# Performance work log

Hardware: AMD Instinct MI355X
Metric: run time of the kernel (lower is better)

Reference implementation:

```python
import jax, jax.numpy as jnp
import numpy as np

N_NODES = 100000
N_EDGES = 1600000
F_IN = 128
F_HID = 128
F_OUT = 128
N_GRAPHS = 256


def setup_inputs() -> dict:
    key = jax.random.key(0)
    ks = jax.random.split(key, 8)
    x = jax.random.normal(ks[0], (N_NODES, F_IN), dtype=jnp.float32)
    edge_index = jax.random.randint(ks[1], (2, N_EDGES), 0, N_NODES, dtype=jnp.int64)
    batch = jnp.sort(jax.random.randint(ks[2], (N_NODES,), 0, N_GRAPHS, dtype=jnp.int64))
    W1 = jax.random.normal(ks[3], (F_IN, F_HID), dtype=jnp.float32) * 0.05
    b1 = jax.random.normal(ks[4], (F_HID,), dtype=jnp.float32) * 0.05
    W2 = jax.random.normal(ks[5], (F_HID, F_OUT), dtype=jnp.float32) * 0.05
    b2 = jax.random.normal(ks[6], (F_OUT,), dtype=jnp.float32) * 0.05
    return {"x": x, "edge_index": edge_index, "batch": batch,
            "W1": W1, "b1": b1, "W2": W2, "b2": b2}


def reference(x, edge_index, batch, W1, b1, W2, b2):
    n = x.shape[0]
    # --- GCNConv (PyG defaults: add self-loops, symmetric normalization) ---
    loop = jnp.arange(n, dtype=edge_index.dtype)
    row = jnp.concatenate([edge_index[0], loop])  # source nodes
    col = jnp.concatenate([edge_index[1], loop])  # target nodes
    ones = jnp.ones_like(col, dtype=x.dtype)
    deg = jax.ops.segment_sum(ones, col, num_segments=n)          # in-degree incl. self-loop
    dinv = jnp.where(deg > 0, jax.lax.rsqrt(deg), 0.0)
    norm = dinv[row] * dinv[col]                                  # [E+N]
    h = x @ W1                                                    # transform first (PyG order)
    msg = h[row] * norm[:, None]                                  # gather + normalize
    agg = jax.ops.segment_sum(msg, col, num_segments=n) + b1      # scatter-add + bias
    h = jax.nn.relu(agg)
    # --- global_mean_pool over graphs ---
    g_ones = jnp.ones((n,), dtype=x.dtype)
    cnt = jax.ops.segment_sum(g_ones, batch, num_segments=N_GRAPHS)
    pooled = jax.ops.segment_sum(h, batch, num_segments=N_GRAPHS)
    pooled = pooled / jnp.clip(cnt, 1.0)[:, None]
    # --- linear + tanh ---
    return jnp.tanh(pooled @ W2 + b2)
```

## Files before the change

kernel.cpp:

```cpp
#include <hip/hip_runtime.h>
#include <math.h>

#define F 128
#define N_GRAPHS 256
#define BK_SHIFT 8
#define BK_NODES 256
#define BK_CAP 6144
#define MAXBK 512
#define SC_CAP 3200
#define NSCAT 512

typedef __attribute__((ext_vector_type(4))) float f32x4;
typedef __attribute__((ext_vector_type(2))) float f32x2;
typedef __attribute__((ext_vector_type(8))) short bf16x8;
typedef __attribute__((ext_vector_type(8))) unsigned short u16x8;

__device__ __forceinline__ unsigned short f2bf(float f) {
    unsigned u = __float_as_uint(f);
    unsigned r = (u + 0x7FFFu + ((u >> 16) & 1u)) >> 16;
    return (unsigned short)r;
}
__device__ __forceinline__ float bf2f(unsigned short u) {
    return __uint_as_float(((unsigned)u) << 16);
}
__device__ __forceinline__ int idxval(const int* raw, int i, bool is32) {
    return is32 ? raw[i] : (int)((const long long*)raw)[i];
}

#if defined(__has_builtin)
#if __has_builtin(__builtin_amdgcn_cvt_pk_f32_fp8) && __has_builtin(__builtin_amdgcn_cvt_pk_fp8_f32)
#define HW_FP8 1
#endif
#endif

__device__ __forceinline__ unsigned char f2fp8(float f) {
#ifdef HW_FP8
    int p = __builtin_amdgcn_cvt_pk_fp8_f32(f, f, 0, false);
    return (unsigned char)(p & 0xFF);
#else
    float a = fabsf(f);
    unsigned s = (f < 0.f) ? 0x80u : 0u;
    if (a >= 448.f) return s | 0x7E;
    if (a < 0.015625f) {
        int m = (int)(a * 512.f + 0.5f);
        return s | (unsigned)m;
    }
    int ex;
    float fr = frexpf(a, &ex);
    int e = ex - 1;
    int q = (int)(a * exp2f((float)(3 - e)) + 0.5f) - 8;
    if (q == 8) { q = 0; e += 1; }
    return s | ((unsigned)(e + 7) << 3) | (unsigned)q;
#endif
}

__device__ __forceinline__ void fp8x16_fma(uint4 v, float w, float* acc) {
#ifdef HW_FP8
    f32x2 p;
    p = __builtin_amdgcn_cvt_pk_f32_fp8((int)v.x, false); acc[0]  += w * p[0]; acc[1]  += w * p[1];
    p = __builtin_amdgcn_cvt_pk_f32_fp8((int)v.x, true);  acc[2]  += w * p[0]; acc[3]  += w * p[1];
    p = __builtin_amdgcn_cvt_pk_f32_fp8((int)v.y, false); acc[4]  += w * p[0]; acc[5]  += w * p[1];
    p = __builtin_amdgcn_cvt_pk_f32_fp8((int)v.y, true);  acc[6]  += w * p[0]; acc[7]  += w * p[1];
    p = __builtin_amdgcn_cvt_pk_f32_fp8((int)v.z, false); acc[8]  += w * p[0]; acc[9]  += w * p[1];
    p = __builtin_amdgcn_cvt_pk_f32_fp8((int)v.z, true);  acc[10] += w * p[0]; acc[11] += w * p[1];
    p = __builtin_amdgcn_cvt_pk_f32_fp8((int)v.w, false); acc[12] += w * p[0]; acc[13] += w * p[1];
    p = __builtin_amdgcn_cvt_pk_f32_fp8((int)v.w, true);  acc[14] += w * p[0]; acc[15] += w * p[1];
#else
    unsigned ww[4] = {v.x, v.y, v.z, v.w};
#pragma unroll
    for (int j = 0; j < 16; ++j) {
        unsigned b = (ww[j >> 2] >> ((j & 3) * 8)) & 0xFF;
        int e = (b >> 3) & 0xF, m = b & 7;
        float val = e ? ldexpf((float)(8 + m), e - 10) : ldexpf((float)m, -9);
        acc[j] += (b & 0x80) ? -(w * val) : (w * val);
    }
#endif
}

__global__ __launch_bounds__(256) void scatter_gemm_kernel(
    const int* __restrict__ ei_raw, int nE,
    const int* __restrict__ batch_raw, int nN,
    const float* __restrict__ x, const float* __restrict__ W1,
    unsigned char* __restrict__ h_f8,
    int* __restrict__ bcursor, int2* __restrict__ tmp, int nBk) {
    extern __shared__ char smem[];
    int t = threadIdx.x;

    if (blockIdx.x < NSCAT) {
        int2* ebuf  = (int2*)smem;
        int*  hist  = (int*)(smem + SC_CAP * 8);
        int*  rbase = hist + MAXBK;
        bool is32 = (batch_raw[nN - 1] != 0);
        int cs = (nE + NSCAT - 1) / NSCAT;
        int e0 = blockIdx.x * cs;
        int e1 = min(nE, e0 + cs);

        for (int s0 = e0; s0 < e1; s0 += SC_CAP) {
            int m = min(SC_CAP, e1 - s0);
            for (int i = t; i < nBk; i += 256) hist[i] = 0;
            __syncthreads();
            for (int i = t; i < m; i += 256) {
                int r = idxval(ei_raw, s0 + i, is32);
                int c = idxval(ei_raw, nE + s0 + i, is32);
                ebuf[i] = make_int2(r, c);
                atomicAdd(&hist[c >> BK_SHIFT], 1);
            }
            __syncthreads();
            for (int i = t; i < nBk; i += 256) {
                int hv = hist[i];
                rbase[i] = hv ? (i * BK_CAP + atomicAdd(&bcursor[i], hv)) : 0;
                hist[i] = 0;
            }
            __syncthreads();
            for (int i = t; i < m; i += 256) {
                int2 e = ebuf[i];
                int b = e.y >> BK_SHIFT;
                int pos = rbase[b] + atomicAdd(&hist[b], 1);
                if (pos < (b + 1) * BK_CAP)
                    tmp[pos] = e;
            }
            __syncthreads();
        }
    } else {
        unsigned short* xs = (unsigned short*)smem;
        unsigned short* wl = (unsigned short*)(smem + 32768);
        int row0 = (blockIdx.x - NSCAT) * 128;

        for (int cch = t; cch < 2048; cch += 256) {
            int n = cch & 127, kc = cch >> 7;
            u16x8 o;
#pragma unroll
            for (int j = 0; j < 8; ++j) o[j] = f2bf(W1[(kc * 8 + j) * F + n]);
            int byte = (n * 256 + kc * 16) ^ ((n & 7) << 4);
            *(u16x8*)((char*)wl + byte) = o;
        }
#pragma unroll
        for (int j = 0; j < 16; ++j) {
            int idx = t + j * 256;
            int r = idx >> 5, c4 = idx & 31;
            int gr = row0 + r;
            float4 v = make_float4(0.f, 0.f, 0.f, 0.f);
            if (gr < nN) v = ((const float4*)x)[(size_t)gr * 32 + c4];
            ushort4 o;
            o.x = f2bf(v.x); o.y = f2bf(v.y); o.z = f2bf(v.z); o.w = f2bf(v.w);
            int byte = (r * 256 + c4 * 8) ^ ((r & 7) << 4);
            *(ushort4*)((char*)xs + byte) = o;
        }
        __syncthreads();

        int lane = t & 63;
        int w = t >> 6;
        int m0 = (w >> 1) * 64;
        int n0 = (w & 1) * 64;
        int l15 = lane & 15;
        int lg = lane >> 4;

        f32x4 acc[4][4] = {};
#pragma unroll
        for (int ks = 0; ks < 4; ++ks) {
            bf16x8 a[4], b[4];
#pragma unroll
            for (int i = 0; i < 4; ++i) {
                int r = m0 + i * 16 + l15;
                int byte = (r * 256 + ks * 64 + lg * 16) ^ ((r & 7) << 4);
                a[i] = *(const bf16x8*)((const char*)xs + byte);
            }
#pragma unroll
            for (int j = 0; j < 4; ++j) {
                int n = n0 + j * 16 + l15;
                int byte = (n * 256 + ks * 64 + lg * 16) ^ ((n & 7) << 4);
                b[j] = *(const bf16x8*)((const char*)wl + byte);
            }
#pragma unroll
            for (int i = 0; i < 4; ++i)
#pragma unroll
                for (int j = 0; j < 4; ++j)
                    acc[i][j] = __builtin_amdgcn_mfma_f32_16x16x32_bf16(
                        a[i], b[j], acc[i][j], 0, 0, 0);
        }

#pragma unroll
        for (int i = 0; i < 4; ++i) {
#pragma unroll
            for (int r = 0; r < 4; ++r) {
                int gm = row0 + m0 + i * 16 + lg * 4 + r;
                if (gm < nN) {
#pragma unroll
                    for (int j = 0; j < 4; ++j) {
                        int n = n0 + j * 16 + l15;
                        h_f8[(size_t)gm * F + n] = f2fp8(acc[i][j][r]);
                    }
                }
            }
        }
    }
}

__global__ __launch_bounds__(256) void bucket_build_kernel(
    const int2* __restrict__ tmp, const int* __restrict__ bfill, int nN,
    int* __restrict__ off, int* __restrict__ cnt, float* __restrict__ dinv,
    int* __restrict__ csr) {
    __shared__ int2 ebuf[BK_CAP];
    __shared__ int h[BK_NODES];
    __shared__ int pfx[BK_NODES];
    __shared__ int lcur[BK_NODES];
    int b = blockIdx.x;
    int t = threadIdx.x;
    int nodeLo = b << BK_SHIFT;
    int base = b * BK_CAP;
    int m = min(bfill[b], BK_CAP);

    h[t] = 0;
    for (int i = t; i < m; i += 256) ebuf[i] = tmp[base + i];
    __syncthreads();
    for (int i = t; i < m; i += 256)
        atomicAdd(&h[ebuf[i].y - nodeLo], 1);
    __syncthreads();
    int own = h[t];
    int pad = (own + 3) & ~3;
    pfx[t] = pad;
    __syncthreads();
    for (int st = 1; st < 256; st <<= 1) {
        int add = (t >= st) ? pfx[t - st] : 0;
        __syncthreads();
        pfx[t] += add;
        __syncthreads();
    }
    int myoff = base + pfx[t] - pad;
    lcur[t] = myoff;
    int node = nodeLo + t;
    if (node < nN) {
        off[node] = myoff;
        cnt[node] = own;
        dinv[node] = rsqrtf((float)(own + 1));
    }
    __syncthreads();
    for (int i = t; i < m; i += 256) {
        int2 e = ebuf[i];
        int pos = atomicAdd(&lcur[e.y - nodeLo], 1);
        csr[pos] = e.x;
    }
}

__global__ __launch_bounds__(256) void aggregate_kernel(
    const unsigned char* __restrict__ h_f8, const int* __restrict__ csr,
    const int* __restrict__ off, const int* __restrict__ cnt,
    const float* __restrict__ dinv, const float* __restrict__ b1,
    unsigned short* __restrict__ agg_bf, int nN) {
    int t = threadIdx.x;
    int lane = t & 7;
    int c = blockIdx.x * 32 + (t >> 3);
    if (c >= nN) return;

    const uint4* h4 = (const uint4*)h_f8;
    int n = cnt[c];
    float dc = rsqrtf((float)(n + 1));
    float acc[16];
#pragma unroll
    for (int j = 0; j < 16; ++j) acc[j] = 0.f;
    fp8x16_fma(h4[(size_t)c * 8 + lane], dc, acc);

    int lo = off[c];
    int k = 0;
    for (; k + 4 <= n; k += 4) {
        int4 e = *(const int4*)(csr + lo + k);
        float w0 = dinv[e.x];
        float w1 = dinv[e.y];
        float w2 = dinv[e.z];
        float w3 = dinv[e.w];
        uint4 v0 = h4[(size_t)e.x * 8 + lane];
        uint4 v1 = h4[(size_t)e.y * 8 + lane];
        uint4 v2 = h4[(size_t)e.z * 8 + lane];
        uint4 v3 = h4[(size_t)e.w * 8 + lane];
        fp8x16_fma(v0, w0, acc);
        fp8x16_fma(v1, w1, acc);
        fp8x16_fma(v2, w2, acc);
        fp8x16_fma(v3, w3, acc);
    }
    if (k < n) {
        int4 e = *(const int4*)(csr + lo + k);
        fp8x16_fma(h4[(size_t)e.x * 8 + lane], dinv[e.x], acc);
        if (k + 1 < n) fp8x16_fma(h4[(size_t)e.y * 8 + lane], dinv[e.y], acc);
        if (k + 2 < n) fp8x16_fma(h4[(size_t)e.z * 8 + lane], dinv[e.z], acc);
    }

    const float* b1p = b1 + lane * 16;
    u16x8 r0, r1;
#pragma unroll
    for (int j = 0; j < 8; ++j) {
        r0[j] = f2bf(fmaxf(b1p[j] + dc * acc[j], 0.f));
        r1[j] = f2bf(fmaxf(b1p[8 + j] + dc * acc[8 + j], 0.f));
    }
    *(u16x8*)(agg_bf + (size_t)c * F + lane * 16) = r0;
    *(u16x8*)(agg_bf + (size_t)c * F + lane * 16 + 8) = r1;
}

__global__ __launch_bounds__(256) void pool_final_kernel(
    const unsigned short* __restrict__ agg_bf,
    const int* __restrict__ batch_raw, int nN,
    const float* __restrict__ W2, const float* __restrict__ b2,
    float* __restrict__ out) {
    int g = blockIdx.x;
    bool is32 = (batch_raw[nN - 1] != 0);
    __shared__ int bounds[2];
    __shared__ float sd[16][F];
    __shared__ float ps[F];
    int t = threadIdx.x;
    if (t < 2) {
        int target = g + t;
        int lo = 0, hi = nN;
        while (lo < hi) {
            int mid = (lo + hi) >> 1;
            if (idxval(batch_raw, mid, is32) < target) lo = mid + 1; else hi = mid;
        }
        bounds[t] = lo;
    }
    __syncthreads();
    int lo = bounds[0], hi = bounds[1];

    int lane = t & 15;
    int grp = t >> 4;
    const u16x8* a8 = (const u16x8*)agg_bf;
    float acc[8];
#pragma unroll
    for (int j = 0; j < 8; ++j) acc[j] = 0.f;
    for (int n = lo + grp; n < hi; n += 16) {
        u16x8 v = a8[(size_t)n * 16 + lane];
#pragma unroll
        for (int j = 0; j < 8; ++j) acc[j] += bf2f(v[j]);
    }
#pragma unroll
    for (int j = 0; j < 8; ++j) sd[grp][lane * 8 + j] = acc[j];
    __syncthreads();

    if (t < F) {
        float s = 0.f;
#pragma unroll
        for (int i = 0; i < 16; ++i) s += sd[i][t];
        float cntf = (float)(hi - lo);
        ps[t] = s / fmaxf(cntf, 1.0f);
    }
    __syncthreads();

    if (t < F) {
        float s = b2[t];
        for (int k = 0; k < F; ++k) s += ps[k] * W2[k * F + t];
        out[g * F + t] = tanhf(s);
    }
}

extern "C" void kernel_launch(void* const* d_in, const int* in_sizes, int n_in,
                              void* d_out, int out_size, void* d_ws, size_t ws_size,
                              hipStream_t stream) {
    const float* x     = (const float*)d_in[0];
    const int*   ei    = (const int*)d_in[1];
    const int*   batch = (const int*)d_in[2];
    const float* W1    = (const float*)d_in[3];
    const float* b1    = (const float*)d_in[4];
    const float* W2    = (const float*)d_in[5];
    const float* b2    = (const float*)d_in[6];
    float* out = (float*)d_out;

    const int nN = in_sizes[2];
    const int nE = in_sizes[1] / 2;
    const int nBk = (nN + BK_NODES - 1) >> BK_SHIFT;
    const int nGemm = (nN + 127) / 128;

    char* ws = (char*)d_ws;
    size_t woff = 0;
    auto take = [&](size_t bytes) {
        void* p = ws + woff;
        woff += (bytes + 15) & ~(size_t)15;
        return p;
    };
    unsigned char*  h_f8   = (unsigned char*)take((size_t)nN * F);
    unsigned short* agg_bf = (unsigned short*)take((size_t)nN * F * 2);
    int2*  tmp      = (int2*)take((size_t)nBk * BK_CAP * 8);
    int*   csr      = (int*)take((size_t)nBk * BK_CAP * 4);
    int*   cnt      = (int*)take((size_t)nN * 4);
    int*   off      = (int*)take((size_t)nN * 4);
    float* dinv     = (float*)take((size_t)nN * 4);
    int*   bcursor  = (int*)take((size_t)nBk * 4);

    hipMemsetAsync(bcursor, 0, (size_t)nBk * 4, stream);
    scatter_gemm_kernel<<<NSCAT + nGemm, 256, 65536, stream>>>(
        ei, nE, batch, nN, x, W1, h_f8, bcursor, tmp, nBk);
    bucket_build_kernel<<<nBk, 256, 0, stream>>>(tmp, bcursor, nN, off, cnt,
                                                 dinv, csr);
    aggregate_kernel<<<(nN + 31) / 32, 256, 0, stream>>>(h_f8, csr, off, cnt,
                                                         dinv, b1, agg_bf, nN);
    pool_final_kernel<<<N_GRAPHS, 256, 0, stream>>>(agg_bf, batch, nN, W2, b2, out);
}
```

Before: 130.3 us.

## Pack bucketed edges into 32-bit words and pretranspose W1 to bf16 once

Each bucketed edge is now one 32-bit word: the source index in the low 20 bits and the target's offset inside its bucket in the high bits. This halves the temp buffer's global traffic and the LDS footprint in the bucket build kernel. W1 is converted to a transposed bf16 copy once by a small new kernel. GEMM blocks then read their B fragments straight from global/L2 instead of each block rebuilding W1 in shared memory, which halves the dynamic LDS request of the fused kernel. The cost is an extra launch, uncoalesced-ish global B loads, and an assumption that node counts fit in 20 bits.

```diff
diff --git a/kernel.cpp b/kernel.cpp
--- a/kernel.cpp
+++ b/kernel.cpp
@@ -77,12 +77,19 @@
 #endif
 }
 
+__global__ __launch_bounds__(256) void w1t_kernel(
+    const float* __restrict__ W1, unsigned short* __restrict__ W1T) {
+    int i = blockIdx.x * 256 + threadIdx.x;
+    int k = i >> 7, n = i & 127;
+    W1T[n * F + k] = f2bf(W1[i]);
+}
+
 __global__ __launch_bounds__(256) void scatter_gemm_kernel(
     const int* __restrict__ ei_raw, int nE,
     const int* __restrict__ batch_raw, int nN,
-    const float* __restrict__ x, const float* __restrict__ W1,
+    const float* __restrict__ x, const unsigned short* __restrict__ W1T,
     unsigned char* __restrict__ h_f8,
-    int* __restrict__ bcursor, int2* __restrict__ tmp, int nBk) {
+    int* __restrict__ bcursor, int* __restrict__ tmp, int nBk) {
     extern __shared__ char smem[];
     int t = threadIdx.x;
 
@@ -117,23 +124,14 @@
                 int b = e.y >> BK_SHIFT;
                 int pos = rbase[b] + atomicAdd(&hist[b], 1);
                 if (pos < (b + 1) * BK_CAP)
-                    tmp[pos] = e;
+                    tmp[pos] = e.x | ((e.y & (BK_NODES - 1)) << 20);
             }
             __syncthreads();
         }
     } else {
         unsigned short* xs = (unsigned short*)smem;
-        unsigned short* wl = (unsigned short*)(smem + 32768);
         int row0 = (blockIdx.x - NSCAT) * 128;
 
-        for (int cch = t; cch < 2048; cch += 256) {
-            int n = cch & 127, kc = cch >> 7;
-            u16x8 o;
-#pragma unroll
-            for (int j = 0; j < 8; ++j) o[j] = f2bf(W1[(kc * 8 + j) * F + n]);
-            int byte = (n * 256 + kc * 16) ^ ((n & 7) << 4);
-            *(u16x8*)((char*)wl + byte) = o;
-        }
 #pragma unroll
         for (int j = 0; j < 16; ++j) {
             int idx = t + j * 256;
@@ -168,8 +166,7 @@
 #pragma unroll
             for (int j = 0; j < 4; ++j) {
                 int n = n0 + j * 16 + l15;
-                int byte = (n * 256 + ks * 64 + lg * 16) ^ ((n & 7) << 4);
-                b[j] = *(const bf16x8*)((const char*)wl + byte);
+                b[j] = *(const bf16x8*)(W1T + (size_t)n * F + ks * 32 + lg * 8);
             }
 #pragma unroll
             for (int i = 0; i < 4; ++i)
@@ -197,10 +194,10 @@
 }
 
 __global__ __launch_bounds__(256) void bucket_build_kernel(
-    const int2* __restrict__ tmp, const int* __restrict__ bfill, int nN,
+    const int* __restrict__ tmp, const int* __restrict__ bfill, int nN,
     int* __restrict__ off, int* __restrict__ cnt, float* __restrict__ dinv,
     int* __restrict__ csr) {
-    __shared__ int2 ebuf[BK_CAP];
+    __shared__ int ebuf[BK_CAP];
     __shared__ int h[BK_NODES];
     __shared__ int pfx[BK_NODES];
     __shared__ int lcur[BK_NODES];
@@ -214,7 +211,7 @@
     for (int i = t; i < m; i += 256) ebuf[i] = tmp[base + i];
     __syncthreads();
     for (int i = t; i < m; i += 256)
-        atomicAdd(&h[ebuf[i].y - nodeLo], 1);
+        atomicAdd(&h[ebuf[i] >> 20], 1);
     __syncthreads();
     int own = h[t];
     int pad = (own + 3) & ~3;
@@ -236,9 +233,9 @@
     }
     __syncthreads();
     for (int i = t; i < m; i += 256) {
-        int2 e = ebuf[i];
-        int pos = atomicAdd(&lcur[e.y - nodeLo], 1);
-        csr[pos] = e.x;
+        int e = ebuf[i];
+        int pos = atomicAdd(&lcur[e >> 20], 1);
+        csr[pos] = e & 0xFFFFF;
     }
 }
 
@@ -375,16 +372,18 @@
     };
     unsigned char*  h_f8   = (unsigned char*)take((size_t)nN * F);
     unsigned short* agg_bf = (unsigned short*)take((size_t)nN * F * 2);
-    int2*  tmp      = (int2*)take((size_t)nBk * BK_CAP * 8);
+    int*   tmp      = (int*)take((size_t)nBk * BK_CAP * 4);
     int*   csr      = (int*)take((size_t)nBk * BK_CAP * 4);
     int*   cnt      = (int*)take((size_t)nN * 4);
     int*   off      = (int*)take((size_t)nN * 4);
     float* dinv     = (float*)take((size_t)nN * 4);
+    unsigned short* W1T = (unsigned short*)take((size_t)F * F * 2);
     int*   bcursor  = (int*)take((size_t)nBk * 4);
 
     hipMemsetAsync(bcursor, 0, (size_t)nBk * 4, stream);
-    scatter_gemm_kernel<<<NSCAT + nGemm, 256, 65536, stream>>>(
-        ei, nE, batch, nN, x, W1, h_f8, bcursor, tmp, nBk);
+    w1t_kernel<<<F * F / 256, 256, 0, stream>>>(W1, W1T);
+    scatter_gemm_kernel<<<NSCAT + nGemm, 256, 32768, stream>>>(
+        ei, nE, batch, nN, x, W1T, h_f8, bcursor, tmp, nBk);
     bucket_build_kernel<<<nBk, 256, 0, stream>>>(tmp, bcursor, nN, off, cnt,
                                                  dinv, csr);
     aggregate_kernel<<<(nN + 31) / 32, 256, 0, stream>>>(h_f8, csr, off, cnt,
```

Result: faster. 122.7 us (-5.9%).
